# Optimization experiments

Hardware: AMD Instinct MI355X
Metric: run time of the kernel (lower is better)

## Reference

```python
import jax, jax.numpy as jnp
import numpy as np
import math

N_HEAD = 16

def setup_inputs() -> dict:
    key = jax.random.key(0)
    ks = jax.random.split(key, 8)
    B, S, P, NX = 4, 1024, 128, 1024
    return {
        "x": jax.random.normal(ks[0], (B, S, NX), jnp.float32),
        "M": jax.random.normal(ks[1], (B, P, NX), jnp.float32),
        "Mmask": jnp.ones((B, P), jnp.float32),
        "attention_mask": jnp.zeros((B, 1, 1, S), jnp.float32),
        "W_attn": jax.random.normal(ks[2], (NX, 3 * NX), jnp.float32) * 0.02,
        "b_attn": jnp.zeros((3 * NX,), jnp.float32),
        "W_mem": jax.random.normal(ks[3], (NX, 2 * NX), jnp.float32) * 0.02,
        "b_mem": jnp.zeros((2 * NX,), jnp.float32),
        "W_proj": jax.random.normal(ks[4], (NX, NX), jnp.float32) * 0.02,
        "b_proj": jnp.zeros((NX,), jnp.float32),
    }

def _split_heads(t, H):
    B, T, NX = t.shape
    return t.reshape(B, T, H, NX // H).transpose(0, 2, 1, 3)  # [B,H,T,dh]

def reference(x, M, Mmask, attention_mask, W_attn, b_attn, W_mem, b_mem, W_proj, b_proj):
    B, S, NX = x.shape
    H = N_HEAD
    dh = NX // H
    P = M.shape[1]

    # fused QKV projection (Conv1D == x @ W + b)
    qkv = x @ W_attn + b_attn
    q, k, v = jnp.split(qkv, 3, axis=2)

    # memory K/V projection, prepended along the key/value sequence axis
    ekv = M @ W_mem + b_mem
    ek, ev = jnp.split(ekv, 2, axis=2)
    key = jnp.concatenate([ek, k], axis=1)   # [B, P+S, NX]
    value = jnp.concatenate([ev, v], axis=1)

    qh = _split_heads(q, H)      # [B,H,S,dh]
    kh = _split_heads(key, H)    # [B,H,P+S,dh]
    vh = _split_heads(value, H)  # [B,H,P+S,dh]

    w = jnp.einsum('bhsd,bhtd->bhst', qh, kh) / math.sqrt(dh)  # [B,H,S,P+S]

    # causal bias over the self part, all-ones over the memory part
    causal = jnp.tril(jnp.ones((S, S), w.dtype))
    b = jnp.concatenate([jnp.ones((S, P), w.dtype), causal], axis=1)[None, None]  # [1,1,S,P+S]
    w = w * b - 10000.0 * (1.0 - b)

    # additive attention mask: memory-mask bias concatenated before token mask
    mem_bias = (1.0 - Mmask)[:, None, None, :] * -10000.0  # [B,1,1,P]
    am = jnp.concatenate([mem_bias, jnp.broadcast_to(attention_mask, (B, 1, 1, S))], axis=3)
    w = w + am

    w = jax.nn.softmax(w, axis=-1)
    a = jnp.einsum('bhst,bhtd->bhsd', w, vh)                  # [B,H,S,dh]
    a = a.transpose(0, 2, 1, 3).reshape(B, S, NX)             # merge heads
    return a @ W_proj + b_proj
```

## Files before the change

### kernel.cpp

```cpp
#include <hip/hip_runtime.h>
#include <hip/hip_bf16.h>


typedef __attribute__((ext_vector_type(8))) short bf16x8;
typedef __attribute__((ext_vector_type(4))) float f32x4;

#define MFMA16(a, b, c) __builtin_amdgcn_mfma_f32_16x16x32_bf16((a), (b), (c), 0, 0, 0)

#define GLOAD_LDS16(g, l)                                                  \
    __builtin_amdgcn_global_load_lds(                                      \
        (const __attribute__((address_space(1))) void*)(const void*)(g),   \
        (__attribute__((address_space(3))) void*)(void*)(l), 16, 0, 0)

static __device__ __forceinline__ unsigned short f2bf(float f) {
    union { float f; unsigned int u; } v; v.f = f;
    unsigned int u = v.u;
    return (unsigned short)((u + 0x7fffu + ((u >> 16) & 1u)) >> 16);
}

static __device__ __forceinline__ void transpose64(const float* __restrict__ W,
                                                   unsigned short* __restrict__ Wt,
                                                   int K, int N, int bx, int by,
                                                   float* tile ) {
    const int n0 = bx * 64, k0 = by * 64;
    const int tr = threadIdx.x >> 2, tc = (threadIdx.x & 3) * 16;
    #pragma unroll
    for (int i = 0; i < 4; i++) {
        float4 v = *(const float4*)&W[(size_t)(k0 + tr) * N + n0 + tc + i * 4];
        tile[tr * 65 + tc + i * 4 + 0] = v.x;
        tile[tr * 65 + tc + i * 4 + 1] = v.y;
        tile[tr * 65 + tc + i * 4 + 2] = v.z;
        tile[tr * 65 + tc + i * 4 + 3] = v.w;
    }
    __syncthreads();
    union { ushort4 u4[2]; unsigned short s[8]; } pk[2];
    #pragma unroll
    for (int half = 0; half < 2; half++)
        #pragma unroll
        for (int i = 0; i < 8; i++)
            pk[half].s[i] = f2bf(tile[(tc + half * 8 + i) * 65 + tr]);
    unsigned short* dst = &Wt[(size_t)(n0 + tr) * K + k0 + tc];
    *(ushort4*)(dst + 0) = pk[0].u4[0];
    *(ushort4*)(dst + 4) = pk[0].u4[1];
    *(ushort4*)(dst + 8) = pk[1].u4[0];
    *(ushort4*)(dst + 12) = pk[1].u4[1];
}

__global__ void prep_all(const float* __restrict__ x, const float* __restrict__ Mem,
                         unsigned short* __restrict__ x_bf, unsigned short* __restrict__ M_bf,
                         const float* __restrict__ W_attn, const float* __restrict__ W_mem,
                         const float* __restrict__ W_proj, unsigned short* __restrict__ Wat,
                         unsigned short* __restrict__ Wmt, unsigned short* __restrict__ Wpt,
                         const float* __restrict__ Mmask, const float* __restrict__ amask,
                         float* __restrict__ biasT) {
    __shared__ float tile[64 * 65];
    int bid = blockIdx.x;
    if (bid < 4608) {
        int i = bid * 256 + threadIdx.x;
        if (i < 1048576) {
            float4 v = ((const float4*)x)[i];
            ushort4 o; o.x = f2bf(v.x); o.y = f2bf(v.y); o.z = f2bf(v.z); o.w = f2bf(v.w);
            ((ushort4*)x_bf)[i] = o;
        } else {
            int j = i - 1048576;
            float4 v = ((const float4*)Mem)[j];
            ushort4 o; o.x = f2bf(v.x); o.y = f2bf(v.y); o.z = f2bf(v.z); o.w = f2bf(v.w);
            ((ushort4*)M_bf)[j] = o;
        }
        return;
    }
    bid -= 4608;
    if (bid < 768) {
        transpose64(W_attn, Wat, 1024, 3072, bid % 48, bid / 48, tile);
    } else if (bid < 1280) {
        int t = bid - 768;  transpose64(W_mem, Wmt, 1024, 2048, t % 32, t / 32, tile);
    } else if (bid < 1536) {
        int t = bid - 1280; transpose64(W_proj, Wpt, 1024, 1024, t % 16, t / 16, tile);
    } else {
        int i = (bid - 1536) * 256 + threadIdx.x;
        if (i < 4 * 1152) {
            int b = i / 1152, t = i % 1152;
            float v = (t < 128) ? (Mmask[b * 128 + t] - 1.f) * 10000.f
                                : amask[b * 1024 + t - 128];
            biasT[i] = v * 1.4426950408889634f;
        }
    }
}

__global__ __launch_bounds__(512, 2) void gemm_fused(
        const unsigned short* __restrict__ x_bf, const unsigned short* __restrict__ Wat,
        const float* __restrict__ b_attn, const unsigned short* __restrict__ M_bf,
        const unsigned short* __restrict__ Wmt, const float* __restrict__ b_mem,
        unsigned short* __restrict__ Qbuf, unsigned short* __restrict__ Kc,
        unsigned short* __restrict__ Vt) {
    __shared__ unsigned short lds[2][32768];
    const int tid = threadIdx.x;
    const int lane = tid & 63, wave = tid >> 6;
    const int quad = lane >> 4, l16 = lane & 15;
    const int l7 = l16 & 7;
    const int srow = lane >> 3;
    const int sblk = (lane & 7) ^ srow;
    const int wrow = wave * 16;
    const int wm = (wave & 1) * 128;
    const int wn = (wave >> 1) * 64;

    int tm, tn;
    const unsigned short *Ab, *Bb;
    const float* bias;
    bool qkv;
    if (blockIdx.x < 192) {
        const int nb = (blockIdx.x & 7) * 24 + (blockIdx.x >> 3);
        tm = nb & 15; tn = nb >> 4;
        Ab = x_bf; Bb = Wat; bias = b_attn; qkv = true;
    } else {
        const int e = blockIdx.x - 192;
        tm = e >> 3; tn = e & 7;
        Ab = M_bf; Bb = Wmt; bias = b_mem; qkv = false;
    }
    const int Mrow0 = tm * 256, Nrow0 = tn * 256;

#define STG(slot, dstoff, srcp, row0, kt1)                                     \
    { _Pragma("unroll")                                                        \
      for (int c = 0; c < 2; c++)                                              \
          GLOAD_LDS16((srcp) + (size_t)((row0) + wrow + c * 8 + srow) * 1024 + \
                          (kt1) * 64 + sblk * 8,                               \
                      &lds[slot][(dstoff) + (wrow + c * 8) * 64]); }

    STG(0, 16384, Bb, Nrow0, 0); STG(0, 24576, Bb, Nrow0 + 128, 0);
    STG(0, 0,     Ab, Mrow0, 0); STG(0, 8192,  Ab, Mrow0 + 128, 0);
    asm volatile("s_waitcnt vmcnt(0)\n\ts_barrier" ::: "memory");

    f32x4 acc[8][4] = {};
    for (int kt = 0; kt < 16; kt++) {
        const int s = kt & 1, nx = s ^ 1;
        bf16x8 bfr[4][2];
        #pragma unroll
        for (int p = 0; p < 4; p++) {
            bf16x8 af[2][2];
            #pragma unroll
            for (int k = 0; k < 2; k++)
                #pragma unroll
                for (int ks = 0; ks < 2; ks++)
                    af[k][ks] = *(const bf16x8*)&lds[s][(wm + (2 * p + k) * 16 + l16) * 64 +
                                                       (((ks * 4 + quad) ^ l7) * 8)];
            if (p == 0) {
                #pragma unroll
                for (int j = 0; j < 4; j++)
                    #pragma unroll
                    for (int ks = 0; ks < 2; ks++)
                        bfr[j][ks] = *(const bf16x8*)&lds[s][16384 + (wn + j * 16 + l16) * 64 +
                                                            (((ks * 4 + quad) ^ l7) * 8)];
            }
            if (kt < 15) {
                if (p == 0) { STG(nx, 16384, Bb, Nrow0, kt + 1);
                              STG(nx, 24576, Bb, Nrow0 + 128, kt + 1); }
                else if (p == 1) { STG(nx, 0,    Ab, Mrow0, kt + 1); }
                else if (p == 2) { STG(nx, 8192, Ab, Mrow0 + 128, kt + 1); }
            }
            if (p == 3) asm volatile("s_waitcnt vmcnt(0)\n\ts_barrier" ::: "memory");
            else        asm volatile("s_barrier" ::: "memory");
            __builtin_amdgcn_s_setprio(1);
            #pragma unroll
            for (int k = 0; k < 2; k++)
                #pragma unroll
                for (int j = 0; j < 4; j++) {
                    acc[2 * p + k][j] = MFMA16(af[k][0], bfr[j][0], acc[2 * p + k][j]);
                    acc[2 * p + k][j] = MFMA16(af[k][1], bfr[j][1], acc[2 * p + k][j]);
                }
            __builtin_amdgcn_s_setprio(0);
            asm volatile("s_barrier" ::: "memory");
        }
    }
#undef STG
    __syncthreads();

    float bj[4];
    #pragma unroll
    for (int j = 0; j < 4; j++) bj[j] = bias[Nrow0 + wn + j * 16 + l16];

    if (qkv) {
        const int b = tm >> 2;
        const int sb = (tm & 3) * 256 + wm;
        if (tn < 4) {
            #pragma unroll
            for (int i = 0; i < 8; i++) {
                const int row = Mrow0 + wm + i * 16 + quad * 4;
                #pragma unroll
                for (int j = 0; j < 4; j++) {
                    const int col = Nrow0 + wn + j * 16 + l16;
                    #pragma unroll
                    for (int r = 0; r < 4; r++)
                        Qbuf[(size_t)(row + r) * 1024 + col] = f2bf(acc[i][j][r] + bj[j]);
                }
            }
        } else if (tn < 8) {
            const int cb = (tn - 4) * 256 + wn;
            unsigned short* kb2 = Kc + (size_t)((b << 4) | (cb >> 6)) * 73728;
            #pragma unroll
            for (int i = 0; i < 8; i++) {
                const int s0 = sb + i * 16 + quad * 4;
                #pragma unroll
                for (int j = 0; j < 4; j++) {
                    const int d = j * 16 + l16;
                    #pragma unroll
                    for (int r = 0; r < 4; r++)
                        kb2[(size_t)(128 + s0 + r) * 64 + d] = f2bf(acc[i][j][r] + bj[j]);
                }
            }
        } else {
            const int vb = (tn - 8) * 256 + wn;
            unsigned short* Tw = &lds[0][0] + wave * 4352;
            unsigned short* vdb = Vt + (size_t)((b << 4) | (vb >> 6)) * 73728;
            #pragma unroll
            for (int hf = 0; hf < 2; hf++) {
                #pragma unroll
                for (int i2 = 0; i2 < 4; i2++)
                    #pragma unroll
                    for (int j = 0; j < 4; j++)
                        #pragma unroll
                        for (int r = 0; r < 4; r++)
                            Tw[(j * 16 + l16) * 68 + i2 * 16 + quad * 4 + r] =
                                f2bf(acc[hf * 4 + i2][j][r] + bj[j]);
                unsigned short* vd = vdb + (size_t)lane * 1152 + 128 + sb + hf * 64;
                #pragma unroll
                for (int ch = 0; ch < 8; ch++)
                    *(bf16x8*)(vd + ch * 8) = *(const bf16x8*)&Tw[lane * 68 + ch * 8];
            }
        }
    } else {
        const int b = (Mrow0 + wm) >> 7;
        if (tn < 4) {
            const int cb = tn * 256 + wn;
            unsigned short* kb2 = Kc + (size_t)((b << 4) | (cb >> 6)) * 73728;
            #pragma unroll
            for (int i = 0; i < 8; i++) {
                const int p0 = i * 16 + quad * 4;
                #pragma unroll
                for (int j = 0; j < 4; j++) {
                    const int d = j * 16 + l16;
                    #pragma unroll
                    for (int r = 0; r < 4; r++)
                        kb2[(size_t)(p0 + r) * 64 + d] = f2bf(acc[i][j][r] + bj[j]);
                }
            }
        } else {
            const int vb = (tn - 4) * 256 + wn;
            unsigned short* Tw = &lds[0][0] + wave * 4352;
            unsigned short* vdb = Vt + (size_t)((b << 4) | (vb >> 6)) * 73728;
            #pragma unroll
            for (int hf = 0; hf < 2; hf++) {
                #pragma unroll
                for (int i2 = 0; i2 < 4; i2++)
                    #pragma unroll
                    for (int j = 0; j < 4; j++)
                        #pragma unroll
                        for (int r = 0; r < 4; r++)
                            Tw[(j * 16 + l16) * 68 + i2 * 16 + quad * 4 + r] =
                                f2bf(acc[hf * 4 + i2][j][r] + bj[j]);
                unsigned short* vd = vdb + (size_t)lane * 1152 + hf * 64;
                #pragma unroll
                for (int ch = 0; ch < 8; ch++)
                    *(bf16x8*)(vd + ch * 8) = *(const bf16x8*)&Tw[lane * 68 + ch * 8];
            }
        }
    }
}

__global__ __launch_bounds__(256) void attn_kernel(const unsigned short* __restrict__ Qbuf,
                                                   const unsigned short* __restrict__ Kc,
                                                   const unsigned short* __restrict__ Vt,
                                                   const float* __restrict__ biasT,
                                                   unsigned short* __restrict__ Aout) {
    __shared__ unsigned short Ks[2][64 * 64];
    __shared__ unsigned short Vs[2][64 * 64];
    __shared__ unsigned short Ps[4][16 * 72];
    const int tid = threadIdx.x;
    const int lane = tid & 63, wave = tid >> 6;
    const int quad = lane >> 4, l16 = lane & 15;
    const int blk = blockIdx.x;
    const int xcd = blk & 7, idx = blk >> 3;
    const int bh = xcd * 8 + (idx & 7);
    const int pair = idx >> 3;
    const int h = bh & 15, b = bh >> 4;

    const unsigned short* Kb = Kc + (size_t)bh * 73728;
    const unsigned short* Vb = Vt + (size_t)bh * 73728;
    const float* bias_b = biasT + b * 1152;

    const int srow = lane >> 3;
    const int scol = ((lane & 7) ^ srow) * 8;
    const int rswz = l16 & 7;
    const int w16 = wave * 16;

#define STAGE_KV(t0_, kdst_, vdst_)                                            \
    {                                                                          \
        const unsigned short* gk = Kb + (size_t)((t0_) + w16 + srow) * 64 + scol; \
        const unsigned short* gv = Vb + (size_t)(w16 + srow) * 1152 + (t0_) + scol; \
        _Pragma("unroll")                                                      \
        for (int cc = 0; cc < 2; cc++) {                                       \
            GLOAD_LDS16(gk + (size_t)(cc * 8) * 64,   &(kdst_)[(w16 + cc * 8) * 64]); \
            GLOAD_LDS16(gv + (size_t)(cc * 8) * 1152, &(vdst_)[(w16 + cc * 8) * 64]); \
        }                                                                      \
    }

    bf16x8 ones;
    #pragma unroll
    for (int j = 0; j < 8; j++) ones[j] = (short)0x3F80;

    #pragma unroll
    for (int phase = 0; phase < 2; phase++) {
        const int qg = phase ? (15 - pair) : pair;
        const int qrow0 = qg * 64;
        const int qrow_w = qrow0 + wave * 16;

        bf16x8 qf[2];
        #pragma unroll
        for (int k2 = 0; k2 < 2; k2++)
            qf[k2] = *(const bf16x8*)(Qbuf + (size_t)(b * 1024 + qrow_w + l16) * 1024 +
                                      h * 64 + k2 * 32 + quad * 8);

        f32x4 o[4] = {};
        f32x4 oden = {};
        const int tmax = min(1152, ((qrow0 + 255) >> 6) << 6);

        STAGE_KV(0, Ks[0], Vs[0]);

        for (int t0 = 0; t0 < tmax; t0 += 64) {
            const int cur = (t0 >> 6) & 1;
            if (t0 + 64 < tmax) {
                if (cur) { STAGE_KV(t0 + 64, Ks[0], Vs[0]); }
                else     { STAGE_KV(t0 + 64, Ks[1], Vs[1]); }
                asm volatile("s_waitcnt vmcnt(4)\n\ts_barrier" ::: "memory");
            } else {
                asm volatile("s_waitcnt vmcnt(0)\n\ts_barrier" ::: "memory");
            }
            if (t0 <= qrow_w + 143) {
                const unsigned short* Kcur = Ks[cur];
                const unsigned short* Vcur = Vs[cur];
                const bool nomask = (t0 + 63 <= 128 + qrow_w);
                float4 bt[4];
                #pragma unroll
                for (int tn = 0; tn < 4; tn++)
                    bt[tn] = *(const float4*)(bias_b + t0 + tn * 16 + quad * 4);
                const int sg = qrow_w + l16;
                #pragma unroll
                for (int tn = 0; tn < 4; tn++) {
                    bf16x8 kf0 = *(const bf16x8*)&Kcur[(tn * 16 + l16) * 64 + (quad ^ rswz) * 8];
                    bf16x8 kf1 = *(const bf16x8*)&Kcur[(tn * 16 + l16) * 64 + ((quad + 4) ^ rswz) * 8];
                    f32x4 st = {};
                    st = MFMA16(kf0, qf[0], st);
                    st = MFMA16(kf1, qf[1], st);
                    float p[4];
                    #pragma unroll
                    for (int r = 0; r < 4; r++) {
                        float e = __builtin_amdgcn_exp2f(st[r] * 0.18033688011112042f + bt[tn][r]);
                        if (!nomask) {
                            const int tg = t0 + tn * 16 + quad * 4 + r;
                            e = (tg < 128 || tg - 128 <= sg) ? e : 0.f;
                        }
                        p[r] = e;
                    }
                    union { ushort4 u; __hip_bfloat162 h2[2]; } pk;
                    pk.h2[0] = __float22bfloat162_rn(float2{p[0], p[1]});
                    pk.h2[1] = __float22bfloat162_rn(float2{p[2], p[3]});
                    *(ushort4*)&Ps[wave][l16 * 72 + tn * 16 + quad * 4] = pk.u;
                }
                #pragma unroll
                for (int tk = 0; tk < 2; tk++) {
                    bf16x8 pf = *(const bf16x8*)&Ps[wave][l16 * 72 + tk * 32 + quad * 8];
                    oden = MFMA16(pf, ones, oden);
                    #pragma unroll
                    for (int dn = 0; dn < 4; dn++) {
                        bf16x8 vf = *(const bf16x8*)&Vcur[(dn * 16 + l16) * 64 +
                                                          ((tk * 4 + quad) ^ rswz) * 8];
                        o[dn] = MFMA16(pf, vf, o[dn]);
                    }
                }
            }
            asm volatile("s_barrier" ::: "memory");
        }

        #pragma unroll
        for (int r = 0; r < 4; r++) {
            const float inv = 1.f / oden[r];
            const size_t orow = (size_t)(b * 1024 + qrow_w + quad * 4 + r) * 1024 + h * 64;
            #pragma unroll
            for (int dn = 0; dn < 4; dn++)
                Aout[orow + dn * 16 + l16] = f2bf(o[dn][r] * inv);
        }
    }
#undef STAGE_KV
}

__global__ __launch_bounds__(512) void gemm_proj(const unsigned short* __restrict__ Abuf,
                                                 const unsigned short* __restrict__ Wpt,
                                                 const float* __restrict__ b_proj,
                                                 float* __restrict__ out) {
    __shared__ unsigned short As[128 * 32];
    __shared__ unsigned short Bs[128 * 32];
    const int tid = threadIdx.x;
    const int lane = tid & 63, wave = tid >> 6;
    const int quad = lane >> 4, l16 = lane & 15;
    const int wm = (wave & 1) * 64, wn = (wave >> 1) * 32;
    const int bm = blockIdx.x & 31, bn = blockIdx.x >> 5;
    const int crow = lane >> 2, ccol = (lane & 3) * 8;
    const unsigned short* Abase = Abuf + (size_t)(bm * 128 + crow) * 1024 + ccol;
    const unsigned short* Bbase = Wpt + (size_t)(bn * 128 + crow) * 1024 + ccol;

    f32x4 acc[4][2] = {};
    for (int k0 = 0; k0 < 1024; k0 += 32) {
        __syncthreads();
        #pragma unroll
        for (int cc = 0; cc < 2; cc++) {
            const int c = wave * 2 + cc;
            if (c < 8) GLOAD_LDS16(Abase + (size_t)(c * 16) * 1024 + k0, &As[c * 512]);
            else       GLOAD_LDS16(Bbase + (size_t)((c - 8) * 16) * 1024 + k0, &Bs[(c - 8) * 512]);
        }
        __syncthreads();
        bf16x8 af[4], bf[2];
        #pragma unroll
        for (int i = 0; i < 4; i++) af[i] = *(const bf16x8*)&As[(wm + i * 16 + l16) * 32 + quad * 8];
        #pragma unroll
        for (int j = 0; j < 2; j++) bf[j] = *(const bf16x8*)&Bs[(wn + j * 16 + l16) * 32 + quad * 8];
        #pragma unroll
        for (int i = 0; i < 4; i++)
            #pragma unroll
            for (int j = 0; j < 2; j++)
                acc[i][j] = MFMA16(af[i], bf[j], acc[i][j]);
    }
    float bj[2];
    #pragma unroll
    for (int j = 0; j < 2; j++) bj[j] = b_proj[bn * 128 + wn + j * 16 + l16];
    #pragma unroll
    for (int i = 0; i < 4; i++) {
        const int row = bm * 128 + wm + i * 16 + quad * 4;
        #pragma unroll
        for (int j = 0; j < 2; j++) {
            const int col = bn * 128 + wn + j * 16 + l16;
            #pragma unroll
            for (int r = 0; r < 4; r++)
                out[(size_t)(row + r) * 1024 + col] = acc[i][j][r] + bj[j];
        }
    }
}

extern "C" void kernel_launch(void* const* d_in, const int* in_sizes, int n_in,
                              void* d_out, int out_size, void* d_ws, size_t ws_size,
                              hipStream_t stream) {
    const float* x      = (const float*)d_in[0];
    const float* Mem    = (const float*)d_in[1];
    const float* Mmask  = (const float*)d_in[2];
    const float* amask  = (const float*)d_in[3];
    const float* W_attn = (const float*)d_in[4];
    const float* b_attn = (const float*)d_in[5];
    const float* W_mem  = (const float*)d_in[6];
    const float* b_mem  = (const float*)d_in[7];
    const float* W_proj = (const float*)d_in[8];
    const float* b_proj = (const float*)d_in[9];
    float* out = (float*)d_out;

    char* ws = (char*)d_ws;
    unsigned short* x_bf  = (unsigned short*)ws;  ws += (size_t)4096 * 1024 * 2;
    unsigned short* M_bf  = (unsigned short*)ws;  ws += (size_t)512 * 1024 * 2;
    unsigned short* Wat   = (unsigned short*)ws;  ws += (size_t)3072 * 1024 * 2;
    unsigned short* Wmt   = (unsigned short*)ws;  ws += (size_t)2048 * 1024 * 2;
    unsigned short* Wpt   = (unsigned short*)ws;  ws += (size_t)1024 * 1024 * 2;
    unsigned short* Qbuf  = (unsigned short*)ws;  ws += (size_t)4096 * 1024 * 2;
    unsigned short* Abuf  = (unsigned short*)ws;  ws += (size_t)4096 * 1024 * 2;
    unsigned short* Kc    = (unsigned short*)ws;  ws += (size_t)64 * 1152 * 64 * 2;
    unsigned short* Vt    = (unsigned short*)ws;  ws += (size_t)64 * 64 * 1152 * 2;
    float*          biasT = (float*)ws;           ws += (size_t)4 * 1152 * 4;

    prep_all<<<6163, 256, 0, stream>>>(x, Mem, x_bf, M_bf, W_attn, W_mem, W_proj,
                                       Wat, Wmt, Wpt, Mmask, amask, biasT);
    gemm_fused<<<208, 512, 0, stream>>>(x_bf, Wat, b_attn, M_bf, Wmt, b_mem,
                                        Qbuf, Kc, Vt);
    attn_kernel<<<512, 256, 0, stream>>>(Qbuf, Kc, Vt, biasT, Abuf);
    gemm_proj<<<256, 512, 0, stream>>>(Abuf, Wpt, b_proj, out);
}
```

Before: 195.5 us.

## Prefetch A fragments one phase ahead and stage Q/K epilogue stores through LDS

Within the QKV/memory projection GEMM, the B fragments and the first A fragments are loaded at the top of each k-step, and the next phase's A fragments are double-buffered in registers so the LDS reads overlap the MFMAs. The Q and K epilogues now go through a per-wave LDS tile, as the V path already did, and write 16-byte vector rows instead of scattered 2-byte stores. This targets LDS read latency in the main loop and uncoalesced global stores in the epilogue. In exchange it uses more registers and adds an LDS round trip in the epilogue.

```diff
diff --git a/kernel.cpp b/kernel.cpp
--- a/kernel.cpp
+++ b/kernel.cpp
@@ -133,30 +133,36 @@
     f32x4 acc[8][4] = {};
     for (int kt = 0; kt < 16; kt++) {
         const int s = kt & 1, nx = s ^ 1;
-        bf16x8 bfr[4][2];
+        bf16x8 bfr[4][2], af[2][2][2];
+        #pragma unroll
+        for (int j = 0; j < 4; j++)
+            #pragma unroll
+            for (int ks = 0; ks < 2; ks++)
+                bfr[j][ks] = *(const bf16x8*)&lds[s][16384 + (wn + j * 16 + l16) * 64 +
+                                                    (((ks * 4 + quad) ^ l7) * 8)];
+        #pragma unroll
+        for (int k = 0; k < 2; k++)
+            #pragma unroll
+            for (int ks = 0; ks < 2; ks++)
+                af[0][k][ks] = *(const bf16x8*)&lds[s][(wm + k * 16 + l16) * 64 +
+                                                       (((ks * 4 + quad) ^ l7) * 8)];
         #pragma unroll
         for (int p = 0; p < 4; p++) {
-            bf16x8 af[2][2];
-            #pragma unroll
-            for (int k = 0; k < 2; k++)
-                #pragma unroll
-                for (int ks = 0; ks < 2; ks++)
-                    af[k][ks] = *(const bf16x8*)&lds[s][(wm + (2 * p + k) * 16 + l16) * 64 +
-                                                       (((ks * 4 + quad) ^ l7) * 8)];
-            if (p == 0) {
-                #pragma unroll
-                for (int j = 0; j < 4; j++)
-                    #pragma unroll
-                    for (int ks = 0; ks < 2; ks++)
-                        bfr[j][ks] = *(const bf16x8*)&lds[s][16384 + (wn + j * 16 + l16) * 64 +
-                                                            (((ks * 4 + quad) ^ l7) * 8)];
-            }
             if (kt < 15) {
                 if (p == 0) { STG(nx, 16384, Bb, Nrow0, kt + 1);
                               STG(nx, 24576, Bb, Nrow0 + 128, kt + 1); }
                 else if (p == 1) { STG(nx, 0,    Ab, Mrow0, kt + 1); }
                 else if (p == 2) { STG(nx, 8192, Ab, Mrow0 + 128, kt + 1); }
             }
+            if (p < 3) {
+                #pragma unroll
+                for (int k = 0; k < 2; k++)
+                    #pragma unroll
+                    for (int ks = 0; ks < 2; ks++)
+                        af[(p + 1) & 1][k][ks] = *(const bf16x8*)&lds[s][
+                            (wm + ((p + 1) * 2 + k) * 16 + l16) * 64 +
+                            (((ks * 4 + quad) ^ l7) * 8)];
+            }
             if (p == 3) asm volatile("s_waitcnt vmcnt(0)\n\ts_barrier" ::: "memory");
             else        asm volatile("s_barrier" ::: "memory");
             __builtin_amdgcn_s_setprio(1);
@@ -164,8 +170,8 @@
             for (int k = 0; k < 2; k++)
                 #pragma unroll
                 for (int j = 0; j < 4; j++) {
-                    acc[2 * p + k][j] = MFMA16(af[k][0], bfr[j][0], acc[2 * p + k][j]);
-                    acc[2 * p + k][j] = MFMA16(af[k][1], bfr[j][1], acc[2 * p + k][j]);
+                    acc[2 * p + k][j] = MFMA16(af[p & 1][k][0], bfr[j][0], acc[2 * p + k][j]);
+                    acc[2 * p + k][j] = MFMA16(af[p & 1][k][1], bfr[j][1], acc[2 * p + k][j]);
                 }
             __builtin_amdgcn_s_setprio(0);
             asm volatile("s_barrier" ::: "memory");
@@ -177,39 +183,44 @@
     float bj[4];
     #pragma unroll
     for (int j = 0; j < 4; j++) bj[j] = bias[Nrow0 + wn + j * 16 + l16];
+
+    unsigned short* Tw = &lds[0][0] + wave * 4352;
+#define TWFILL(hf)                                                             \
+    { _Pragma("unroll")                                                        \
+      for (int i2 = 0; i2 < 4; i2++)                                           \
+          _Pragma("unroll")                                                    \
+          for (int j = 0; j < 4; j++)                                          \
+              _Pragma("unroll")                                                \
+              for (int r = 0; r < 4; r++)                                      \
+                  Tw[(i2 * 16 + quad * 4 + r) * 68 + j * 16 + l16] =           \
+                      f2bf(acc[(hf) * 4 + i2][j][r] + bj[j]); }
 
     if (qkv) {
         const int b = tm >> 2;
         const int sb = (tm & 3) * 256 + wm;
         if (tn < 4) {
             #pragma unroll
-            for (int i = 0; i < 8; i++) {
-                const int row = Mrow0 + wm + i * 16 + quad * 4;
-                #pragma unroll
-                for (int j = 0; j < 4; j++) {
-                    const int col = Nrow0 + wn + j * 16 + l16;
-                    #pragma unroll
-                    for (int r = 0; r < 4; r++)
-                        Qbuf[(size_t)(row + r) * 1024 + col] = f2bf(acc[i][j][r] + bj[j]);
-                }
+            for (int hf = 0; hf < 2; hf++) {
+                TWFILL(hf);
+                unsigned short* qd = Qbuf + (size_t)(Mrow0 + wm + hf * 64 + lane) * 1024 +
+                                     Nrow0 + wn;
+                #pragma unroll
+                for (int ch = 0; ch < 8; ch++)
+                    *(bf16x8*)(qd + ch * 8) = *(const bf16x8*)&Tw[lane * 68 + ch * 8];
             }
         } else if (tn < 8) {
             const int cb = (tn - 4) * 256 + wn;
             unsigned short* kb2 = Kc + (size_t)((b << 4) | (cb >> 6)) * 73728;
             #pragma unroll
-            for (int i = 0; i < 8; i++) {
-                const int s0 = sb + i * 16 + quad * 4;
-                #pragma unroll
-                for (int j = 0; j < 4; j++) {
-                    const int d = j * 16 + l16;
-                    #pragma unroll
-                    for (int r = 0; r < 4; r++)
-                        kb2[(size_t)(128 + s0 + r) * 64 + d] = f2bf(acc[i][j][r] + bj[j]);
-                }
+            for (int hf = 0; hf < 2; hf++) {
+                TWFILL(hf);
+                unsigned short* kd = kb2 + (size_t)(128 + sb + hf * 64 + lane) * 64;
+                #pragma unroll
+                for (int ch = 0; ch < 8; ch++)
+                    *(bf16x8*)(kd + ch * 8) = *(const bf16x8*)&Tw[lane * 68 + ch * 8];
             }
         } else {
             const int vb = (tn - 8) * 256 + wn;
-            unsigned short* Tw = &lds[0][0] + wave * 4352;
             unsigned short* vdb = Vt + (size_t)((b << 4) | (vb >> 6)) * 73728;
             #pragma unroll
             for (int hf = 0; hf < 2; hf++) {
@@ -233,19 +244,15 @@
             const int cb = tn * 256 + wn;
             unsigned short* kb2 = Kc + (size_t)((b << 4) | (cb >> 6)) * 73728;
             #pragma unroll
-            for (int i = 0; i < 8; i++) {
-                const int p0 = i * 16 + quad * 4;
-                #pragma unroll
-                for (int j = 0; j < 4; j++) {
-                    const int d = j * 16 + l16;
-                    #pragma unroll
-                    for (int r = 0; r < 4; r++)
-                        kb2[(size_t)(p0 + r) * 64 + d] = f2bf(acc[i][j][r] + bj[j]);
-                }
+            for (int hf = 0; hf < 2; hf++) {
+                TWFILL(hf);
+                unsigned short* kd = kb2 + (size_t)(hf * 64 + lane) * 64;
+                #pragma unroll
+                for (int ch = 0; ch < 8; ch++)
+                    *(bf16x8*)(kd + ch * 8) = *(const bf16x8*)&Tw[lane * 68 + ch * 8];
             }
         } else {
             const int vb = (tn - 4) * 256 + wn;
-            unsigned short* Tw = &lds[0][0] + wave * 4352;
             unsigned short* vdb = Vt + (size_t)((b << 4) | (vb >> 6)) * 73728;
             #pragma unroll
             for (int hf = 0; hf < 2; hf++) {
@@ -264,6 +271,7 @@
             }
         }
     }
+#undef TWFILL
 }
 
 __global__ __launch_bounds__(256) void attn_kernel(const unsigned short* __restrict__ Qbuf,
```

After: 195.1 us. About the same (-0.2%).

## Deepen QKV/mem GEMM prefetch to two k-tiles ahead within the double buffer

Applied to the files above, without the earlier changes.

Restructures the projection GEMM's software pipeline. Global-to-LDS loads now run up to two k-tiles ahead: stage-0 chunks are rewritten into the current slot as soon as their fragments have been read into registers. All A fragments for phases 2 and 3 are read from LDS early at p==2, which frees the slot region for reuse. The waits become partial (vmcnt(6)) so more loads stay in flight during the MFMAs. This costs more registers and relies on subtle ordering of reads, barriers and waits for correctness.

```diff
diff --git a/kernel.cpp b/kernel.cpp
--- a/kernel.cpp
+++ b/kernel.cpp
@@ -128,21 +128,16 @@
 
     STG(0, 16384, Bb, Nrow0, 0); STG(0, 24576, Bb, Nrow0 + 128, 0);
     STG(0, 0,     Ab, Mrow0, 0); STG(0, 8192,  Ab, Mrow0 + 128, 0);
-    asm volatile("s_waitcnt vmcnt(0)\n\ts_barrier" ::: "memory");
+    STG(1, 16384, Bb, Nrow0, 1); STG(1, 24576, Bb, Nrow0 + 128, 1);
+    STG(1, 0,     Ab, Mrow0, 1);
+    asm volatile("s_waitcnt vmcnt(6)\n\ts_barrier" ::: "memory");
 
     f32x4 acc[8][4] = {};
     for (int kt = 0; kt < 16; kt++) {
         const int s = kt & 1, nx = s ^ 1;
-        bf16x8 bfr[4][2];
+        bf16x8 bfr[4][2], af[4][2][2];
         #pragma unroll
         for (int p = 0; p < 4; p++) {
-            bf16x8 af[2][2];
-            #pragma unroll
-            for (int k = 0; k < 2; k++)
-                #pragma unroll
-                for (int ks = 0; ks < 2; ks++)
-                    af[k][ks] = *(const bf16x8*)&lds[s][(wm + (2 * p + k) * 16 + l16) * 64 +
-                                                       (((ks * 4 + quad) ^ l7) * 8)];
             if (p == 0) {
                 #pragma unroll
                 for (int j = 0; j < 4; j++)
@@ -151,21 +146,42 @@
                         bfr[j][ks] = *(const bf16x8*)&lds[s][16384 + (wn + j * 16 + l16) * 64 +
                                                             (((ks * 4 + quad) ^ l7) * 8)];
             }
-            if (kt < 15) {
-                if (p == 0) { STG(nx, 16384, Bb, Nrow0, kt + 1);
-                              STG(nx, 24576, Bb, Nrow0 + 128, kt + 1); }
-                else if (p == 1) { STG(nx, 0,    Ab, Mrow0, kt + 1); }
-                else if (p == 2) { STG(nx, 8192, Ab, Mrow0 + 128, kt + 1); }
-            }
-            if (p == 3) asm volatile("s_waitcnt vmcnt(0)\n\ts_barrier" ::: "memory");
-            else        asm volatile("s_barrier" ::: "memory");
+            if (p < 2) {
+                #pragma unroll
+                for (int k = 0; k < 2; k++)
+                    #pragma unroll
+                    for (int ks = 0; ks < 2; ks++)
+                        af[p][k][ks] = *(const bf16x8*)&lds[s][
+                            (wm + (2 * p + k) * 16 + l16) * 64 +
+                            (((ks * 4 + quad) ^ l7) * 8)];
+            } else if (p == 2) {
+                #pragma unroll
+                for (int pp = 2; pp < 4; pp++)
+                    #pragma unroll
+                    for (int k = 0; k < 2; k++)
+                        #pragma unroll
+                        for (int ks = 0; ks < 2; ks++)
+                            af[pp][k][ks] = *(const bf16x8*)&lds[s][
+                                (wm + (2 * pp + k) * 16 + l16) * 64 +
+                                (((ks * 4 + quad) ^ l7) * 8)];
+            }
+            if (p == 0)      { if (kt < 15) STG(nx, 8192,  Ab, Mrow0 + 128, kt + 1); }
+            else if (p == 1) { if (kt < 14) STG(s,  16384, Bb, Nrow0,       kt + 2); }
+            else if (p == 2) { if (kt < 14) STG(s,  24576, Bb, Nrow0 + 128, kt + 2); }
+            else             { if (kt < 14) STG(s,  0,     Ab, Mrow0,       kt + 2); }
+            if (p == 3) {
+                if (kt < 14) asm volatile("s_waitcnt vmcnt(6)\n\ts_barrier" ::: "memory");
+                else         asm volatile("s_waitcnt vmcnt(0)\n\ts_barrier" ::: "memory");
+            } else {
+                asm volatile("s_barrier" ::: "memory");
+            }
             __builtin_amdgcn_s_setprio(1);
             #pragma unroll
             for (int k = 0; k < 2; k++)
                 #pragma unroll
                 for (int j = 0; j < 4; j++) {
-                    acc[2 * p + k][j] = MFMA16(af[k][0], bfr[j][0], acc[2 * p + k][j]);
-                    acc[2 * p + k][j] = MFMA16(af[k][1], bfr[j][1], acc[2 * p + k][j]);
+                    acc[2 * p + k][j] = MFMA16(af[p][k][0], bfr[j][0], acc[2 * p + k][j]);
+                    acc[2 * p + k][j] = MFMA16(af[p][k][1], bfr[j][1], acc[2 * p + k][j]);
                 }
             __builtin_amdgcn_s_setprio(0);
             asm volatile("s_barrier" ::: "memory");
```

Result: no change. 194.4 us (-0.6%).
